# Performance work log

Hardware: AMD Instinct MI355X
Metric: run time of the kernel (lower is better)

## Reference

```python
import jax, jax.numpy as jnp
import numpy as np

EMB = 1024
HID = 2048
N_EXPERTS = 8
CAPACITY_FACTOR = 1.25
Z_LOSS_COEFF = 0.001


def setup_inputs() -> dict:
    key = jax.random.key(0)
    ks = jax.random.split(key, 8)
    B, T = 8, 4096
    x = jax.random.normal(ks[0], (B, T, EMB), dtype=jnp.float32)
    s_r = 1.0 / np.sqrt(EMB)
    s_h = 1.0 / np.sqrt(HID)
    wr = jax.random.uniform(ks[1], (EMB, N_EXPERTS), jnp.float32, -s_r, s_r)
    br = jax.random.uniform(ks[2], (N_EXPERTS,), jnp.float32, -s_r, s_r)
    w1 = jax.random.uniform(ks[3], (N_EXPERTS, EMB, HID), jnp.float32, -s_r, s_r)
    b1 = jax.random.uniform(ks[4], (N_EXPERTS, HID), jnp.float32, -s_r, s_r)
    w2 = jax.random.uniform(ks[5], (N_EXPERTS, HID, EMB), jnp.float32, -s_h, s_h)
    b2 = jax.random.uniform(ks[6], (N_EXPERTS, EMB), jnp.float32, -s_h, s_h)
    return {"x": x, "wr": wr, "br": br, "w1": w1, "b1": b1, "w2": w2, "b2": b2, "k": 2}


def reference(x, wr, br, w1, b1, w2, b2, k):
    B, T, D = x.shape
    E = wr.shape[1]
    N = B * T
    cap = int(CAPACITY_FACTOR * N / E)

    # Router
    logits = jnp.einsum("btd,de->bte", x, wr) + br
    probs = jax.nn.softmax(logits, axis=-1)
    z_loss = Z_LOSS_COEFF * jnp.mean(logits * logits)
    _, topk_idx = jax.lax.top_k(probs, k)  # [B,T,k]

    xf = x.reshape(N, D)
    idx = topk_idx.reshape(N, k)

    # mask[e, n]: token n routed to expert e (any of its top-k slots)
    mask = (idx[None, :, :] == jnp.arange(E, dtype=idx.dtype)[:, None, None]).any(-1)
    pos = jnp.cumsum(mask.astype(jnp.int32), axis=1) - 1  # rank within expert (flattened order)
    keep = mask & (pos < cap)  # capacity truncation: keep first `cap` tokens per expert

    # buf[e, c] = flat index of c-th kept token for expert e, or N (pad)
    cols = jnp.where(keep, pos, cap)  # dropped/unrouted tokens go to dump column
    rows = jnp.broadcast_to(jnp.arange(E)[:, None], (E, N))
    toks_id = jnp.broadcast_to(jnp.arange(N, dtype=jnp.int32)[None, :], (E, N))
    buf = jnp.full((E, cap + 1), N, dtype=jnp.int32).at[rows, cols].set(toks_id)[:, :cap]

    # Dispatch (gather), per-expert dense FFN, combine (scatter-add)
    x_pad = jnp.concatenate([xf, jnp.zeros((1, D), x.dtype)], axis=0)
    toks = x_pad[buf]  # [E, cap, D]
    h = jax.nn.gelu(jnp.einsum("ecd,edh->ech", toks, w1) + b1[:, None, :], approximate=False)
    out = jnp.einsum("ech,ehd->ecd", h, w2) + b2[:, None, :]  # [E, cap, D]
    out_flat = jnp.zeros((N + 1, D), x.dtype).at[buf.reshape(-1)].add(out.reshape(-1, D))[:N]
    output = out_flat.reshape(B, T, D)

    expert_usage = keep.sum(axis=1).astype(jnp.float32)  # [E]
    load = expert_usage / (expert_usage.sum() + 1e-6)
    balance_loss = E * jnp.sum(load * load)
    return output, balance_loss + z_loss, expert_usage
```

## Files before the change

### kernel.cpp

```cpp
#include <hip/hip_runtime.h>
#include <cstdint>

#define NTOK   32768
#define EMB_D  1024
#define HID_H  2048
#define NEXP   8
#define CAP    5120
#define MROWS  (NEXP * CAP)
#define NCHUNK 32

typedef __bf16 bf16_t;
typedef bf16_t bf16x8 __attribute__((ext_vector_type(8)));
typedef float  f32x4  __attribute__((ext_vector_type(4)));

typedef __attribute__((address_space(3))) void       lds_void_t;
typedef const __attribute__((address_space(1))) void g_void_t;

__device__ __forceinline__ void gload_lds16(const void* g, void* l) {
    __builtin_amdgcn_global_load_lds((g_void_t*)(uintptr_t)g,
                                     (lds_void_t*)(uint32_t)(uintptr_t)l, 16, 0, 0);
}

__global__ void router_kernel(const float* __restrict__ x, const float* __restrict__ wr,
                              const float* __restrict__ br, int2* __restrict__ top2,
                              float* __restrict__ zsum) {
    __shared__ float s_wr[NEXP * EMB_D];
    __shared__ float s_z[4];
    const int tid = threadIdx.x;
    for (int i = tid; i < NEXP * EMB_D; i += 256) {
        int d = i >> 3, e = i & 7;
        s_wr[e * EMB_D + d] = wr[i];
    }
    __syncthreads();
    const int wid = tid >> 6, lane = tid & 63;
    const int t = blockIdx.x * 4 + wid;
    const float* xr = x + (size_t)t * EMB_D;

    float acc[NEXP];
#pragma unroll
    for (int e = 0; e < NEXP; e++) acc[e] = 0.f;
#pragma unroll
    for (int it = 0; it < EMB_D / 64; ++it) {
        float xv = xr[lane + 64 * it];
#pragma unroll
        for (int e = 0; e < NEXP; e++) acc[e] += xv * s_wr[e * EMB_D + lane + 64 * it];
    }
#pragma unroll
    for (int e = 0; e < NEXP; e++) {
        float v = acc[e];
#pragma unroll
        for (int off = 32; off > 0; off >>= 1) v += __shfl_xor(v, off);
        acc[e] = v;
    }
    if (lane == 0) {
        float lg[NEXP]; float zs = 0.f;
#pragma unroll
        for (int e = 0; e < NEXP; e++) { lg[e] = acc[e] + br[e]; zs += lg[e] * lg[e]; }
        s_z[wid] = zs;
        float mx = lg[0];
        for (int e = 1; e < NEXP; e++) mx = fmaxf(mx, lg[e]);
        float p[NEXP]; float se = 0.f;
        for (int e = 0; e < NEXP; e++) { p[e] = expf(lg[e] - mx); se += p[e]; }
        for (int e = 0; e < NEXP; e++) p[e] = p[e] / se;
        int i0 = 0; float b0 = p[0];
        for (int e = 1; e < NEXP; e++) if (p[e] > b0) { b0 = p[e]; i0 = e; }
        int i1 = -1; float b1v = -1.f;
        for (int e = 0; e < NEXP; e++) if (e != i0 && p[e] > b1v) { b1v = p[e]; i1 = e; }
        top2[t] = make_int2(i0, i1);
    }
    __syncthreads();
    if (tid == 0) unsafeAtomicAdd(zsum, s_z[0] + s_z[1] + s_z[2] + s_z[3]);
}

__global__ void count_kernel(const int2* __restrict__ top2, int* __restrict__ counts) {
    const int chunk = blockIdx.x;
    const int tid = threadIdx.x;
    const int wid = tid >> 6, lane = tid & 63;
    __shared__ int wcnt[NEXP][16];
    const int2 tp = top2[chunk * 1024 + tid];
#pragma unroll
    for (int e = 0; e < NEXP; e++) {
        const bool m = (tp.x == e) || (tp.y == e);
        unsigned long long bal = __ballot(m);
        if (lane == 0) wcnt[e][wid] = __popcll(bal);
    }
    __syncthreads();
    if (tid < NEXP) {
        int s = 0;
        for (int w = 0; w < 16; w++) s += wcnt[tid][w];
        counts[chunk * NEXP + tid] = s;
    }
}

__global__ void prefix_kernel(const int* __restrict__ counts, int* __restrict__ base,
                              int* __restrict__ usage) {
    const int e = threadIdx.x;
    if (e < NEXP) {
        int run = 0;
        for (int c = 0; c < NCHUNK; c++) {
            base[c * NEXP + e] = run;
            run += counts[c * NEXP + e];
        }
        usage[e] = run < CAP ? run : CAP;
    }
}

__global__ void place_kernel(const int2* __restrict__ top2, const int* __restrict__ base,
                             int* __restrict__ buf, int* __restrict__ inv) {
    const int chunk = blockIdx.x;
    const int tid = threadIdx.x;
    const int wid = tid >> 6, lane = tid & 63;
    const int t = chunk * 1024 + tid;
    __shared__ int wpre[NEXP][16];
    const int2 tp = top2[t];
    int lpre[NEXP]; bool mm[NEXP];
#pragma unroll
    for (int e = 0; e < NEXP; e++) {
        mm[e] = (tp.x == e) || (tp.y == e);
        unsigned long long bal = __ballot(mm[e]);
        lpre[e] = __popcll(bal & ((1ull << lane) - 1ull));
        if (lane == 0) wpre[e][wid] = __popcll(bal);
    }
    __syncthreads();
    if (tid < NEXP) {
        int a = 0;
        for (int w = 0; w < 16; w++) { int v = wpre[tid][w]; wpre[tid][w] = a; a += v; }
    }
    __syncthreads();
#pragma unroll
    for (int e = 0; e < NEXP; e++) {
        if (mm[e]) {
            const int pos = base[chunk * NEXP + e] + wpre[e][wid] + lpre[e];
            const int slot = (tp.x == e) ? 0 : 1;
            if (pos < CAP) {
                const int row = e * CAP + pos;
                buf[row] = t;
                inv[t * 2 + slot] = row;
            } else {
                inv[t * 2 + slot] = -1;
            }
        }
    }
}

__global__ void pad_kernel(const int* __restrict__ usage, int* __restrict__ buf) {
    const int e = blockIdx.x;
    const int u = usage[e];
    for (int p = u + threadIdx.x; p < CAP; p += blockDim.x) buf[e * CAP + p] = NTOK;
}

__global__ void gather_kernel(const float* __restrict__ x, const int* __restrict__ buf,
                              bf16_t* __restrict__ Xg) {
    const int row = blockIdx.x;
    const int t = buf[row];
    const int tid = threadIdx.x;
    bf16x8 v;
    if (t >= 0 && t < NTOK) {
        const float* xr = x + (size_t)t * EMB_D + tid * 8;
        const float4 a = *(const float4*)(xr);
        const float4 b = *(const float4*)(xr + 4);
        v[0] = (bf16_t)a.x; v[1] = (bf16_t)a.y; v[2] = (bf16_t)a.z; v[3] = (bf16_t)a.w;
        v[4] = (bf16_t)b.x; v[5] = (bf16_t)b.y; v[6] = (bf16_t)b.z; v[7] = (bf16_t)b.w;
    } else {
#pragma unroll
        for (int i = 0; i < 8; i++) v[i] = (bf16_t)0.f;
    }
    *(bf16x8*)(Xg + (size_t)row * EMB_D + tid * 8) = v;
}

__global__ void transpose_conv_kernel(const float* __restrict__ in, bf16_t* __restrict__ out,
                                      int R, int C) {
    __shared__ bf16_t tile[64][72];
    const int e = blockIdx.z;
    const int c0 = blockIdx.x * 64, r0 = blockIdx.y * 64;
    const float*  ip = in  + (size_t)e * R * C;
    bf16_t*       op = out + (size_t)e * R * C;
    const int tid = threadIdx.x;
    const int tr = tid >> 4;
    const int tc = (tid & 15) * 4;
#pragma unroll
    for (int rr = 0; rr < 64; rr += 16) {
        const float4 v = *(const float4*)(ip + (size_t)(r0 + tr + rr) * C + (c0 + tc));
        tile[tr + rr][tc + 0] = (bf16_t)v.x;
        tile[tr + rr][tc + 1] = (bf16_t)v.y;
        tile[tr + rr][tc + 2] = (bf16_t)v.z;
        tile[tr + rr][tc + 3] = (bf16_t)v.w;
    }
    __syncthreads();
    const int oc = tid >> 2;
    const int og = (tid & 3) * 16;
    bf16x8 v0, v1;
#pragma unroll
    for (int i = 0; i < 8; i++) v0[i] = tile[og + i][oc];
#pragma unroll
    for (int i = 0; i < 8; i++) v1[i] = tile[og + 8 + i][oc];
    *(bf16x8*)(op + (size_t)(c0 + oc) * R + r0 + og)     = v0;
    *(bf16x8*)(op + (size_t)(c0 + oc) * R + r0 + og + 8) = v1;
}

__device__ __forceinline__ void mfma_mainloop(const bf16_t* __restrict__ Ap,
                                              const bf16_t* __restrict__ Bp,
                                              int K, bf16_t* ldsA, bf16_t* ldsB,
                                              f32x4 (&acc)[4][4]) {
    const int tid = threadIdx.x;
    const int wid = tid >> 6, lane = tid & 63;
    const int wm = wid >> 1, wn = wid & 1;
    const int quad = lane >> 4, l16 = lane & 15;
    const int s0 = tid, s1 = 256 + tid;
    const int row0 = s0 >> 2, ko0 = (s0 & 3) * 8;
    const int row1 = s1 >> 2, ko1 = (s1 & 3) * 8;

    for (int k0 = 0; k0 < K; k0 += 32) {
        __syncthreads();
        gload_lds16(Ap + (size_t)row0 * K + k0 + ko0, ldsA + s0 * 8);
        gload_lds16(Ap + (size_t)row1 * K + k0 + ko1, ldsA + s1 * 8);
        gload_lds16(Bp + (size_t)row0 * K + k0 + ko0, ldsB + s0 * 8);
        gload_lds16(Bp + (size_t)row1 * K + k0 + ko1, ldsB + s1 * 8);
        __builtin_amdgcn_s_waitcnt(0);
        __syncthreads();

        bf16x8 af[4], bfr[4];
#pragma unroll
        for (int i = 0; i < 4; i++) {
            af[i]  = *(const bf16x8*)(ldsA + (wm * 64 + i * 16 + l16) * 32 + quad * 8);
            bfr[i] = *(const bf16x8*)(ldsB + (wn * 64 + i * 16 + l16) * 32 + quad * 8);
        }
#pragma unroll
        for (int i = 0; i < 4; i++)
#pragma unroll
            for (int j = 0; j < 4; j++)
                acc[i][j] = __builtin_amdgcn_mfma_f32_16x16x32_bf16(af[i], bfr[j], acc[i][j], 0, 0, 0);
    }
}

__global__ void gemm1_kernel(const bf16_t* __restrict__ Xg, const bf16_t* __restrict__ w1t,
                             const float* __restrict__ b1, bf16_t* __restrict__ H) {
    __shared__ bf16_t ldsA[128 * 32];
    __shared__ bf16_t ldsB[128 * 32];
    const int bn = blockIdx.x, bm = blockIdx.y;
    const int e = bm / (CAP / 128);
    const bf16_t* Ap = Xg + (size_t)bm * 128 * EMB_D;
    const bf16_t* Bp = w1t + ((size_t)e * HID_H + bn * 128) * EMB_D;
    f32x4 acc[4][4];
    const f32x4 z4 = {0.f, 0.f, 0.f, 0.f};
#pragma unroll
    for (int i = 0; i < 4; i++)
#pragma unroll
        for (int j = 0; j < 4; j++) acc[i][j] = z4;

    mfma_mainloop(Ap, Bp, EMB_D, ldsA, ldsB, acc);

    const int tid = threadIdx.x;
    const int wid = tid >> 6, lane = tid & 63;
    const int wm = wid >> 1, wn = wid & 1;
    const int quad = lane >> 4, l16 = lane & 15;
#pragma unroll
    for (int j = 0; j < 4; j++) {
        const int col = bn * 128 + wn * 64 + j * 16 + l16;
        const float bias = b1[e * HID_H + col];
#pragma unroll
        for (int i = 0; i < 4; i++) {
            const int rowb = bm * 128 + wm * 64 + i * 16 + quad * 4;
#pragma unroll
            for (int r = 0; r < 4; r++) {
                const float v = acc[i][j][r] + bias;
                const float g = 0.5f * v * (1.f + erff(v * 0.7071067811865475f));
                H[(size_t)(rowb + r) * HID_H + col] = (bf16_t)g;
            }
        }
    }
}

__global__ void gemm2_kernel(const bf16_t* __restrict__ H, const bf16_t* __restrict__ w2t,
                             bf16_t* __restrict__ Yg) {
    __shared__ bf16_t ldsA[128 * 32];
    __shared__ bf16_t ldsB[128 * 32];
    const int bn = blockIdx.x, bm = blockIdx.y;
    const int e = bm / (CAP / 128);
    const bf16_t* Ap = H + (size_t)bm * 128 * HID_H;
    const bf16_t* Bp = w2t + ((size_t)e * EMB_D + bn * 128) * HID_H;
    f32x4 acc[4][4];
    const f32x4 z4 = {0.f, 0.f, 0.f, 0.f};
#pragma unroll
    for (int i = 0; i < 4; i++)
#pragma unroll
        for (int j = 0; j < 4; j++) acc[i][j] = z4;

    mfma_mainloop(Ap, Bp, HID_H, ldsA, ldsB, acc);

    const int tid = threadIdx.x;
    const int wid = tid >> 6, lane = tid & 63;
    const int wm = wid >> 1, wn = wid & 1;
    const int quad = lane >> 4, l16 = lane & 15;
#pragma unroll
    for (int j = 0; j < 4; j++) {
        const int col = bn * 128 + wn * 64 + j * 16 + l16;
#pragma unroll
        for (int i = 0; i < 4; i++) {
            const int rowb = bm * 128 + wm * 64 + i * 16 + quad * 4;
#pragma unroll
            for (int r = 0; r < 4; r++)
                Yg[(size_t)(rowb + r) * EMB_D + col] = (bf16_t)acc[i][j][r];
        }
    }
}

__global__ void combine_kernel(const bf16_t* __restrict__ Yg, const float* __restrict__ b2,
                               const int* __restrict__ inv, float* __restrict__ out) {
    const int t = blockIdx.x;
    const int tid = threadIdx.x;
    const int d = tid * 8;
    const int r0 = inv[t * 2], r1 = inv[t * 2 + 1];
    float acc[8];
#pragma unroll
    for (int i = 0; i < 8; i++) acc[i] = 0.f;
    if (r0 >= 0) {
        const int e = r0 / CAP;
        const bf16x8 v = *(const bf16x8*)(Yg + (size_t)r0 * EMB_D + d);
        const float* bp = b2 + e * EMB_D + d;
#pragma unroll
        for (int i = 0; i < 8; i++) acc[i] += (float)v[i] + bp[i];
    }
    if (r1 >= 0) {
        const int e = r1 / CAP;
        const bf16x8 v = *(const bf16x8*)(Yg + (size_t)r1 * EMB_D + d);
        const float* bp = b2 + e * EMB_D + d;
#pragma unroll
        for (int i = 0; i < 8; i++) acc[i] += (float)v[i] + bp[i];
    }
    float4 o0 = {acc[0], acc[1], acc[2], acc[3]};
    float4 o1 = {acc[4], acc[5], acc[6], acc[7]};
    *(float4*)(out + (size_t)t * EMB_D + d)     = o0;
    *(float4*)(out + (size_t)t * EMB_D + d + 4) = o1;
}

__global__ void finalize_kernel(const int* __restrict__ usage, const float* __restrict__ zsum,
                                float* __restrict__ out) {
    if (threadIdx.x == 0) {
        float u[NEXP], s = 0.f;
        for (int e = 0; e < NEXP; e++) { u[e] = (float)usage[e]; s += u[e]; }
        const float inv = 1.f / (s + 1e-6f);
        float bal = 0.f;
        for (int e = 0; e < NEXP; e++) { const float l = u[e] * inv; bal += l * l; }
        bal *= (float)NEXP;
        const float z = 0.001f * zsum[0] / (float)((size_t)NTOK * NEXP);
        out[(size_t)NTOK * EMB_D] = bal + z;
        for (int e = 0; e < NEXP; e++) out[(size_t)NTOK * EMB_D + 1 + e] = u[e];
    }
}

extern "C" void kernel_launch(void* const* d_in, const int* in_sizes, int n_in,
                              void* d_out, int out_size, void* d_ws, size_t ws_size,
                              hipStream_t stream) {
    (void)in_sizes; (void)n_in; (void)out_size;
    const float* x  = (const float*)d_in[0];
    const float* wr = (const float*)d_in[1];
    const float* br = (const float*)d_in[2];
    const float* w1 = (const float*)d_in[3];
    const float* b1 = (const float*)d_in[4];
    const float* w2 = (const float*)d_in[5];
    const float* b2 = (const float*)d_in[6];
    float* out = (float*)d_out;

    uint8_t* ws = (uint8_t*)d_ws;
    size_t off = 0;
    auto carve = [&](size_t bytes) -> void* {
        off = (off + 255) & ~(size_t)255;
        void* p = ws + off;
        off += bytes;
        return p;
    };
    float*  zsum  = (float*)carve(sizeof(float));
    int*    usage = (int*)carve(NEXP * sizeof(int));
    int*    counts = (int*)carve((size_t)NCHUNK * NEXP * sizeof(int));
    int*    base   = (int*)carve((size_t)NCHUNK * NEXP * sizeof(int));
    int2*   top2 = (int2*)carve((size_t)NTOK * sizeof(int2));
    int*    buf  = (int*)carve((size_t)MROWS * sizeof(int));
    int*    inv  = (int*)carve((size_t)NTOK * 2 * sizeof(int));
    bf16_t* Xg   = (bf16_t*)carve((size_t)MROWS * EMB_D * sizeof(bf16_t));
    bf16_t* w1t  = (bf16_t*)carve((size_t)NEXP * HID_H * EMB_D * sizeof(bf16_t));
    bf16_t* w2t  = (bf16_t*)carve((size_t)NEXP * EMB_D * HID_H * sizeof(bf16_t));
    bf16_t* H    = (bf16_t*)carve((size_t)MROWS * HID_H * sizeof(bf16_t));
    bf16_t* Yg   = Xg;
    if (off > ws_size) return;

    hipMemsetAsync(zsum, 0, sizeof(float), stream);

    router_kernel<<<NTOK / 4, 256, 0, stream>>>(x, wr, br, top2, zsum);
    count_kernel<<<NCHUNK, 1024, 0, stream>>>(top2, counts);
    prefix_kernel<<<1, 64, 0, stream>>>(counts, base, usage);
    place_kernel<<<NCHUNK, 1024, 0, stream>>>(top2, base, buf, inv);
    pad_kernel<<<NEXP, 256, 0, stream>>>(usage, buf);
    gather_kernel<<<MROWS, 128, 0, stream>>>(x, buf, Xg);
    transpose_conv_kernel<<<dim3(HID_H / 64, EMB_D / 64, NEXP), 256, 0, stream>>>(w1, w1t, EMB_D, HID_H);
    transpose_conv_kernel<<<dim3(EMB_D / 64, HID_H / 64, NEXP), 256, 0, stream>>>(w2, w2t, HID_H, EMB_D);
    gemm1_kernel<<<dim3(HID_H / 128, MROWS / 128), 256, 0, stream>>>(Xg, w1t, b1, H);
    gemm2_kernel<<<dim3(EMB_D / 128, MROWS / 128), 256, 0, stream>>>(H, w2t, Yg);
    combine_kernel<<<NTOK, 128, 0, stream>>>(Yg, b2, inv, out);
    finalize_kernel<<<1, 64, 0, stream>>>(usage, zsum, out);
}
```

Before: 970.2 us.

## Rewrite expert GEMMs with 256x256 tiles and double-buffered swizzled LDS pipeline

```diff
diff --git a/kernel.cpp b/kernel.cpp
--- a/kernel.cpp
+++ b/kernel.cpp
@@ -198,109 +198,204 @@
     *(bf16x8*)(op + (size_t)(c0 + oc) * R + r0 + og + 8) = v1;
 }
 
-__device__ __forceinline__ void mfma_mainloop(const bf16_t* __restrict__ Ap,
-                                              const bf16_t* __restrict__ Bp,
-                                              int K, bf16_t* ldsA, bf16_t* ldsB,
-                                              f32x4 (&acc)[4][4]) {
-    const int tid = threadIdx.x;
-    const int wid = tid >> 6, lane = tid & 63;
-    const int wm = wid >> 1, wn = wid & 1;
+#define BUF_BYTES 65536
+#define LDS_TOTAL 131072
+
+__device__ __forceinline__ const bf16x8* fragp(const char* base, int row, int ks, int quad) {
+    int b = row * 128 + ks * 64 + quad * 16;
+    b ^= ((b >> 9) & 1) << 5;
+    return (const bf16x8*)(base + b);
+}
+
+__device__ __forceinline__ void stage_ht(const bf16_t* __restrict__ Ap,
+                                         const bf16_t* __restrict__ Bp,
+                                         int K, int NT, char* lds0, int idx,
+                                         size_t off0, int tid) {
+    if (idx >= 4 * NT) return;
+    const int t = idx >> 2, part = idx & 3;
+    char* dst = lds0 + (t & 1) * BUF_BYTES + ((part < 2) ? 32768 : 0)
+              + (part & 1) * 16384 + tid * 16;
+    const bf16_t* src = ((part < 2) ? Bp : Ap)
+                      + (size_t)((part & 1) * 128) * K + (size_t)t * 64 + off0;
+    gload_lds16(src, dst);
+    gload_lds16(src + (size_t)64 * K, dst + 8192);
+}
+
+template <int NT>
+__device__ __forceinline__ void mainloop256(const bf16_t* __restrict__ Ap,
+                                            const bf16_t* __restrict__ Bp,
+                                            char* lds0, f32x4 (&acc)[8][4]) {
+    const int K = NT * 64;
+    const int tid = threadIdx.x;
+    const int lane = tid & 63, wid = tid >> 6;
+    const int wm = wid >> 2, wn = wid & 3;
     const int quad = lane >> 4, l16 = lane & 15;
-    const int s0 = tid, s1 = 256 + tid;
-    const int row0 = s0 >> 2, ko0 = (s0 & 3) * 8;
-    const int row1 = s1 >> 2, ko1 = (s1 & 3) * 8;
-
-    for (int k0 = 0; k0 < K; k0 += 32) {
-        __syncthreads();
-        gload_lds16(Ap + (size_t)row0 * K + k0 + ko0, ldsA + s0 * 8);
-        gload_lds16(Ap + (size_t)row1 * K + k0 + ko1, ldsA + s1 * 8);
-        gload_lds16(Bp + (size_t)row0 * K + k0 + ko0, ldsB + s0 * 8);
-        gload_lds16(Bp + (size_t)row1 * K + k0 + ko1, ldsB + s1 * 8);
-        __builtin_amdgcn_s_waitcnt(0);
-        __syncthreads();
-
-        bf16x8 af[4], bfr[4];
-#pragma unroll
-        for (int i = 0; i < 4; i++) {
-            af[i]  = *(const bf16x8*)(ldsA + (wm * 64 + i * 16 + l16) * 32 + quad * 8);
-            bfr[i] = *(const bf16x8*)(ldsB + (wn * 64 + i * 16 + l16) * 32 + quad * 8);
-        }
-#pragma unroll
-        for (int i = 0; i < 4; i++)
-#pragma unroll
-            for (int j = 0; j < 4; j++)
-                acc[i][j] = __builtin_amdgcn_mfma_f32_16x16x32_bf16(af[i], bfr[j], acc[i][j], 0, 0, 0);
-    }
-}
-
-__global__ void gemm1_kernel(const bf16_t* __restrict__ Xg, const bf16_t* __restrict__ w1t,
-                             const float* __restrict__ b1, bf16_t* __restrict__ H) {
-    __shared__ bf16_t ldsA[128 * 32];
-    __shared__ bf16_t ldsB[128 * 32];
+
+    const int o0 = tid * 16;
+    const int lg = o0 ^ (((o0 >> 9) & 1) << 5);
+    const size_t off0 = (size_t)(lg >> 7) * K + ((lg & 127) >> 1);
+
+#pragma unroll
+    for (int idx = 0; idx < 6; ++idx) stage_ht(Ap, Bp, K, NT, lds0, idx, off0, tid);
+    asm volatile("s_waitcnt vmcnt(4)");
+    __builtin_amdgcn_s_barrier();
+
+    bf16x8 a[8], bl[4], bh[4];
+    for (int t = 0; t < NT; ++t) {
+        const char* bufA = lds0 + (t & 1) * BUF_BYTES;
+        const char* bufB = bufA + 32768;
+        const int pbase = 4 * t + 6;
+
+#pragma unroll
+        for (int mf = 0; mf < 4; ++mf)
+#pragma unroll
+            for (int ks = 0; ks < 2; ++ks)
+                a[mf * 2 + ks] = *fragp(bufA, wm * 128 + mf * 16 + l16, ks, quad);
+#pragma unroll
+        for (int nf = 0; nf < 2; ++nf)
+#pragma unroll
+            for (int ks = 0; ks < 2; ++ks)
+                bl[nf * 2 + ks] = *fragp(bufB, wn * 64 + nf * 16 + l16, ks, quad);
+        stage_ht(Ap, Bp, K, NT, lds0, pbase + 0, off0, tid);
+        __builtin_amdgcn_s_barrier();
+        asm volatile("s_waitcnt lgkmcnt(0)");
+        __builtin_amdgcn_s_setprio(1);
+#pragma unroll
+        for (int mf = 0; mf < 4; ++mf)
+#pragma unroll
+            for (int nf = 0; nf < 2; ++nf)
+#pragma unroll
+                for (int ks = 0; ks < 2; ++ks)
+                    acc[mf][nf] = __builtin_amdgcn_mfma_f32_16x16x32_bf16(
+                        a[mf * 2 + ks], bl[nf * 2 + ks], acc[mf][nf], 0, 0, 0);
+        __builtin_amdgcn_s_setprio(0);
+        __builtin_amdgcn_s_barrier();
+
+#pragma unroll
+        for (int nf = 0; nf < 2; ++nf)
+#pragma unroll
+            for (int ks = 0; ks < 2; ++ks)
+                bh[nf * 2 + ks] = *fragp(bufB, wn * 64 + (nf + 2) * 16 + l16, ks, quad);
+        stage_ht(Ap, Bp, K, NT, lds0, pbase + 1, off0, tid);
+        __builtin_amdgcn_s_barrier();
+        asm volatile("s_waitcnt lgkmcnt(0)");
+        __builtin_amdgcn_s_setprio(1);
+#pragma unroll
+        for (int mf = 0; mf < 4; ++mf)
+#pragma unroll
+            for (int nf = 0; nf < 2; ++nf)
+#pragma unroll
+                for (int ks = 0; ks < 2; ++ks)
+                    acc[mf][nf + 2] = __builtin_amdgcn_mfma_f32_16x16x32_bf16(
+                        a[mf * 2 + ks], bh[nf * 2 + ks], acc[mf][nf + 2], 0, 0, 0);
+        __builtin_amdgcn_s_setprio(0);
+        __builtin_amdgcn_s_barrier();
+
+#pragma unroll
+        for (int mf = 0; mf < 4; ++mf)
+#pragma unroll
+            for (int ks = 0; ks < 2; ++ks)
+                a[mf * 2 + ks] = *fragp(bufA, wm * 128 + (mf + 4) * 16 + l16, ks, quad);
+        stage_ht(Ap, Bp, K, NT, lds0, pbase + 2, off0, tid);
+        __builtin_amdgcn_s_barrier();
+        asm volatile("s_waitcnt lgkmcnt(0)");
+        __builtin_amdgcn_s_setprio(1);
+#pragma unroll
+        for (int mf = 0; mf < 4; ++mf)
+#pragma unroll
+            for (int nf = 0; nf < 2; ++nf)
+#pragma unroll
+                for (int ks = 0; ks < 2; ++ks)
+                    acc[mf + 4][nf + 2] = __builtin_amdgcn_mfma_f32_16x16x32_bf16(
+                        a[mf * 2 + ks], bh[nf * 2 + ks], acc[mf + 4][nf + 2], 0, 0, 0);
+        __builtin_amdgcn_s_setprio(0);
+        __builtin_amdgcn_s_barrier();
+
+        stage_ht(Ap, Bp, K, NT, lds0, pbase + 3, off0, tid);
+        __builtin_amdgcn_s_setprio(1);
+#pragma unroll
+        for (int mf = 0; mf < 4; ++mf)
+#pragma unroll
+            for (int nf = 0; nf < 2; ++nf)
+#pragma unroll
+                for (int ks = 0; ks < 2; ++ks)
+                    acc[mf + 4][nf] = __builtin_amdgcn_mfma_f32_16x16x32_bf16(
+                        a[mf * 2 + ks], bl[nf * 2 + ks], acc[mf + 4][nf], 0, 0, 0);
+        __builtin_amdgcn_s_setprio(0);
+        asm volatile("s_waitcnt vmcnt(4)");
+        __builtin_amdgcn_s_barrier();
+    }
+}
+
+__global__ __launch_bounds__(512, 2) void gemm1_kernel(const bf16_t* __restrict__ Xg,
+                                                       const bf16_t* __restrict__ w1t,
+                                                       const float* __restrict__ b1,
+                                                       bf16_t* __restrict__ H) {
+    extern __shared__ char lds0[];
     const int bn = blockIdx.x, bm = blockIdx.y;
-    const int e = bm / (CAP / 128);
-    const bf16_t* Ap = Xg + (size_t)bm * 128 * EMB_D;
-    const bf16_t* Bp = w1t + ((size_t)e * HID_H + bn * 128) * EMB_D;
-    f32x4 acc[4][4];
+    const int e = bm / (CAP / 256);
+    const bf16_t* Ap = Xg + (size_t)bm * 256 * EMB_D;
+    const bf16_t* Bp = w1t + ((size_t)e * HID_H + bn * 256) * EMB_D;
+    f32x4 acc[8][4];
     const f32x4 z4 = {0.f, 0.f, 0.f, 0.f};
 #pragma unroll
-    for (int i = 0; i < 4; i++)
+    for (int i = 0; i < 8; i++)
 #pragma unroll
         for (int j = 0; j < 4; j++) acc[i][j] = z4;
 
-    mfma_mainloop(Ap, Bp, EMB_D, ldsA, ldsB, acc);
-
-    const int tid = threadIdx.x;
-    const int wid = tid >> 6, lane = tid & 63;
-    const int wm = wid >> 1, wn = wid & 1;
+    mainloop256<EMB_D / 64>(Ap, Bp, lds0, acc);
+
+    const int tid = threadIdx.x;
+    const int lane = tid & 63, wid = tid >> 6;
+    const int wm = wid >> 2, wn = wid & 3;
     const int quad = lane >> 4, l16 = lane & 15;
 #pragma unroll
-    for (int j = 0; j < 4; j++) {
-        const int col = bn * 128 + wn * 64 + j * 16 + l16;
+    for (int nf = 0; nf < 4; ++nf) {
+        const int col = bn * 256 + wn * 64 + nf * 16 + l16;
         const float bias = b1[e * HID_H + col];
 #pragma unroll
-        for (int i = 0; i < 4; i++) {
-            const int rowb = bm * 128 + wm * 64 + i * 16 + quad * 4;
-#pragma unroll
-            for (int r = 0; r < 4; r++) {
-                const float v = acc[i][j][r] + bias;
+        for (int mf = 0; mf < 8; ++mf) {
+            const int row = bm * 256 + wm * 128 + mf * 16 + quad * 4;
+#pragma unroll
+            for (int r = 0; r < 4; ++r) {
+                const float v = acc[mf][nf][r] + bias;
                 const float g = 0.5f * v * (1.f + erff(v * 0.7071067811865475f));
-                H[(size_t)(rowb + r) * HID_H + col] = (bf16_t)g;
+                H[(size_t)(row + r) * HID_H + col] = (bf16_t)g;
             }
         }
     }
 }
 
-__global__ void gemm2_kernel(const bf16_t* __restrict__ H, const bf16_t* __restrict__ w2t,
-                             bf16_t* __restrict__ Yg) {
-    __shared__ bf16_t ldsA[128 * 32];
-    __shared__ bf16_t ldsB[128 * 32];
+__global__ __launch_bounds__(512, 2) void gemm2_kernel(const bf16_t* __restrict__ H,
+                                                       const bf16_t* __restrict__ w2t,
+                                                       bf16_t* __restrict__ Yg) {
+    extern __shared__ char lds0[];
     const int bn = blockIdx.x, bm = blockIdx.y;
-    const int e = bm / (CAP / 128);
-    const bf16_t* Ap = H + (size_t)bm * 128 * HID_H;
-    const bf16_t* Bp = w2t + ((size_t)e * EMB_D + bn * 128) * HID_H;
-    f32x4 acc[4][4];
+    const int e = bm / (CAP / 256);
+    const bf16_t* Ap = H + (size_t)bm * 256 * HID_H;
+    const bf16_t* Bp = w2t + ((size_t)e * EMB_D + bn * 256) * HID_H;
+    f32x4 acc[8][4];
     const f32x4 z4 = {0.f, 0.f, 0.f, 0.f};
 #pragma unroll
-    for (int i = 0; i < 4; i++)
+    for (int i = 0; i < 8; i++)
 #pragma unroll
         for (int j = 0; j < 4; j++) acc[i][j] = z4;
 
-    mfma_mainloop(Ap, Bp, HID_H, ldsA, ldsB, acc);
-
-    const int tid = threadIdx.x;
-    const int wid = tid >> 6, lane = tid & 63;
-    const int wm = wid >> 1, wn = wid & 1;
+    mainloop256<HID_H / 64>(Ap, Bp, lds0, acc);
+
+    const int tid = threadIdx.x;
+    const int lane = tid & 63, wid = tid >> 6;
+    const int wm = wid >> 2, wn = wid & 3;
     const int quad = lane >> 4, l16 = lane & 15;
 #pragma unroll
-    for (int j = 0; j < 4; j++) {
-        const int col = bn * 128 + wn * 64 + j * 16 + l16;
-#pragma unroll
-        for (int i = 0; i < 4; i++) {
-            const int rowb = bm * 128 + wm * 64 + i * 16 + quad * 4;
-#pragma unroll
-            for (int r = 0; r < 4; r++)
-                Yg[(size_t)(rowb + r) * EMB_D + col] = (bf16_t)acc[i][j][r];
+    for (int nf = 0; nf < 4; ++nf) {
+        const int col = bn * 256 + wn * 64 + nf * 16 + l16;
+#pragma unroll
+        for (int mf = 0; mf < 8; ++mf) {
+            const int row = bm * 256 + wm * 128 + mf * 16 + quad * 4;
+#pragma unroll
+            for (int r = 0; r < 4; ++r)
+                Yg[(size_t)(row + r) * EMB_D + col] = (bf16_t)acc[mf][nf][r];
         }
     }
 }
@@ -384,6 +479,15 @@
     bf16_t* Yg   = Xg;
     if (off > ws_size) return;
 
+    static bool attr_set = false;
+    if (!attr_set) {
+        hipFuncSetAttribute(reinterpret_cast<const void*>(&gemm1_kernel),
+                            hipFuncAttributeMaxDynamicSharedMemorySize, LDS_TOTAL);
+        hipFuncSetAttribute(reinterpret_cast<const void*>(&gemm2_kernel),
+                            hipFuncAttributeMaxDynamicSharedMemorySize, LDS_TOTAL);
+        attr_set = true;
+    }
+
     hipMemsetAsync(zsum, 0, sizeof(float), stream);
 
     router_kernel<<<NTOK / 4, 256, 0, stream>>>(x, wr, br, top2, zsum);
@@ -394,8 +498,8 @@
     gather_kernel<<<MROWS, 128, 0, stream>>>(x, buf, Xg);
     transpose_conv_kernel<<<dim3(HID_H / 64, EMB_D / 64, NEXP), 256, 0, stream>>>(w1, w1t, EMB_D, HID_H);
     transpose_conv_kernel<<<dim3(EMB_D / 64, HID_H / 64, NEXP), 256, 0, stream>>>(w2, w2t, HID_H, EMB_D);
-    gemm1_kernel<<<dim3(HID_H / 128, MROWS / 128), 256, 0, stream>>>(Xg, w1t, b1, H);
-    gemm2_kernel<<<dim3(EMB_D / 128, MROWS / 128), 256, 0, stream>>>(H, w2t, Yg);
+    gemm1_kernel<<<dim3(HID_H / 256, MROWS / 256), 512, LDS_TOTAL, stream>>>(Xg, w1t, b1, H);
+    gemm2_kernel<<<dim3(EMB_D / 256, MROWS / 256), 512, LDS_TOTAL, stream>>>(H, w2t, Yg);
     combine_kernel<<<NTOK, 128, 0, stream>>>(Yg, b2, inv, out);
     finalize_kernel<<<1, 64, 0, stream>>>(usage, zsum, out);
 }
```

Result: no change. 953.3 us (-1.7%).
